# Kernel optimization log

Hardware: AMD Instinct MI355X
Metric: run time of the kernel (lower is better)

The kernel has to match this reference:

```python
import jax, jax.numpy as jnp
import numpy as np

N = 100000   # total nodes in batch
E = 200000   # total edges
G = 4000     # number of graphs
H = 128      # gin_size = gin_hidden = gin_mlp_hidden = linear_hidden
L = 2        # gin_layers


def setup_inputs() -> dict:
    key = jax.random.key(0)
    ks = jax.random.split(key, 24)
    rn = lambda i, shape, s=0.05: (jax.random.normal(ks[i], shape, jnp.float32) * s)
    inp = dict(
        x=rn(0, (N, 14), 1.0),
        edge_attr=rn(1, (E, 4), 1.0),
        edge_index=jax.random.randint(ks[2], (2, E), 0, N, dtype=jnp.int32),
        batch=jnp.sort(jax.random.randint(ks[3], (N,), 0, G, dtype=jnp.int32)),
        node_w=rn(4, (14, H)), node_b=jnp.zeros((H,), jnp.float32),
        edge_w=rn(5, (4, H)), edge_b=jnp.zeros((H,), jnp.float32),
        eps=jnp.zeros((L,), jnp.float32),
        gin_w1=rn(6, (L, H, H)), gin_b1=jnp.zeros((L, H), jnp.float32),
        gin_w2=rn(7, (L, H, H)), gin_b2=jnp.zeros((L, H), jnp.float32),
        em_w1=rn(8, (L, H, H)), em_b1=jnp.zeros((L, H), jnp.float32),
        em_w2=rn(9, (L, H, H)), em_b2=jnp.zeros((L, H), jnp.float32),
        gru_wih=rn(10, (3 * H, H)), gru_whh=rn(11, (3 * H, H)),
        gru_bih=jnp.zeros((3 * H,), jnp.float32), gru_bhh=jnp.zeros((3 * H,), jnp.float32),
        lstm_wih=rn(12, (4 * H, 2 * H)), lstm_whh=rn(13, (4 * H, H)),
        lstm_bih=jnp.zeros((4 * H,), jnp.float32), lstm_bhh=jnp.zeros((4 * H,), jnp.float32),
        fc_w1=rn(14, (2 * H, H)), fc_b1=jnp.zeros((H,), jnp.float32),
        fc_w2=rn(15, (H, 1)), fc_b2=jnp.zeros((1,), jnp.float32),
    )
    return inp


def reference(x, edge_attr, edge_index, batch,
              node_w, node_b, edge_w, edge_b, eps,
              gin_w1, gin_b1, gin_w2, gin_b2,
              em_w1, em_b1, em_w2, em_b2,
              gru_wih, gru_whh, gru_bih, gru_bhh,
              lstm_wih, lstm_whh, lstm_bih, lstm_bhh,
              fc_w1, fc_b1, fc_w2, fc_b2):
    src, dst = edge_index[0], edge_index[1]
    node = x @ node_w + node_b          # [N,H]
    edge = edge_attr @ edge_w + edge_b  # [E,H]
    h = node                            # GRU hidden state
    for l in range(L):
        # GINEConv: msg = relu(x_src + e), scatter-add to dst, (1+eps)*x + agg, then MLP
        msg = jax.nn.relu(node[src] + edge)                     # [E,H] gather
        agg = jax.ops.segment_sum(msg, dst, num_segments=N)     # [N,H] scatter-add
        z = (1.0 + eps[l]) * node + agg
        m = jax.nn.relu(z @ gin_w1[l] + gin_b1[l]) @ gin_w2[l] + gin_b2[l]
        # GRU cell (seq_len=1)
        gi = m @ gru_wih.T + gru_bih
        gh = h @ gru_whh.T + gru_bhh
        ir, iz, inn = jnp.split(gi, 3, axis=-1)
        hr, hz, hn = jnp.split(gh, 3, axis=-1)
        r = jax.nn.sigmoid(ir + hr)
        zt = jax.nn.sigmoid(iz + hz)
        n = jnp.tanh(inn + r * hn)
        h = (1.0 - zt) * n + zt * h
        node = h
        # edge feature update MLP
        edge = jax.nn.relu(edge @ em_w1[l] + em_b1[l]) @ em_w2[l] + em_b2[l]
    # Set2Set pooling, processing_steps=3
    qs = jnp.zeros((G, 2 * H), node.dtype)
    hl = jnp.zeros((G, H), node.dtype)
    cl = jnp.zeros((G, H), node.dtype)
    for _ in range(3):
        g = qs @ lstm_wih.T + lstm_bih + hl @ lstm_whh.T + lstm_bhh
        i_, f_, g_, o_ = jnp.split(g, 4, axis=-1)
        cl = jax.nn.sigmoid(f_) * cl + jax.nn.sigmoid(i_) * jnp.tanh(g_)
        hl = jax.nn.sigmoid(o_) * jnp.tanh(cl)
        q = hl                                                   # [G,H]
        e = jnp.sum(node * q[batch], axis=-1)                    # [N]
        emax = jax.ops.segment_max(e, batch, num_segments=G)
        ex = jnp.exp(e - emax[batch])
        denom = jax.ops.segment_sum(ex, batch, num_segments=G)
        a = ex / jnp.maximum(denom, 1e-9)[batch]                 # per-graph softmax
        r = jax.ops.segment_sum(a[:, None] * node, batch, num_segments=G)  # [G,H]
        qs = jnp.concatenate([q, r], axis=-1)                    # [G,2H]
    out = jax.nn.relu(qs @ fc_w1 + fc_b1) @ fc_w2 + fc_b2
    return out.reshape(-1)
```

## Files before the change

### kernel.cpp

```cpp
#include <hip/hip_runtime.h>
#include <hip/hip_bf16.h>

constexpr int TN = 100000;
constexpr int TE = 200000;
constexpr int TG = 4000;
constexpr int TH = 128;

using short8 = __attribute__((ext_vector_type(8))) short;
using f32x4  = __attribute__((ext_vector_type(4))) float;
typedef __hip_bfloat16 bf16;

#define DEVINL __device__ __forceinline__
DEVINL float sigm(float x)  { return 1.f / (1.f + __expf(-x)); }
DEVINL float ftanh(float x) { return 1.f - 2.f / (__expf(2.f * x) + 1.f); }
DEVINL void unpack8(uint4 v, float* f) {
    const ushort* u = (const ushort*)&v;
#pragma unroll
    for (int j = 0; j < 8; ++j) f[j] = __bfloat162float(*(const bf16*)&u[j]);
}

__global__ void conv6(const float* __restrict__ s0, const float* __restrict__ s1,
                      const float* __restrict__ s2, const float* __restrict__ s3,
                      const float* __restrict__ s4, const float* __restrict__ s5,
                      bf16* __restrict__ dst) {
    int i = blockIdx.x * 256 + threadIdx.x;
    if (i >= 6 * TH * TH) return;
    int m = i >> 14, r = i & 16383;
    int n = r >> 7, k = r & 127;
    const float* s = (m == 0) ? s0 : (m == 1) ? s1 : (m == 2) ? s2
                   : (m == 3) ? s3 : (m == 4) ? s4 : s5;
    dst[i] = __float2bfloat16(s[k * TH + n]);
}
__global__ void conv2(const float* __restrict__ a, const float* __restrict__ b,
                      bf16* __restrict__ dst) {
    int i = blockIdx.x * 256 + threadIdx.x;
    if (i >= 2 * 384 * TH) return;
    const float* s = (i < 384 * TH) ? a : b;
    int r = (i < 384 * TH) ? i : i - 384 * TH;
    dst[i] = __float2bfloat16(s[r]);
}
__global__ void convL(const float* __restrict__ wih, const float* __restrict__ whh,
                      bf16* __restrict__ dst) {
    int i = blockIdx.x * 256 + threadIdx.x;
    if (i >= 512 * 256) return;
    int c = i >> 8, k = i & 255;
    float v = (k < 128) ? wih[c * 256 + k] + whh[c * 128 + k] : wih[c * 256 + k];
    dst[i] = __float2bfloat16(v);
}

template<int K>
__global__ __launch_bounds__(256) void proj64(const float* __restrict__ X,
                                              const float* __restrict__ W,
                                              const float* __restrict__ b,
                                              ushort* __restrict__ out, int M) {
    __shared__ float xs[64][K];
    int tid = threadIdx.x;
    int bm = blockIdx.x * 64;
    for (int i = tid; i < 64 * K; i += 256) {
        int r = i / K, k = i % K;
        xs[r][k] = (bm + r < M) ? X[(size_t)(bm + r) * K + k] : 0.f;
    }
    __syncthreads();
    int rb = tid >> 4, h0 = (tid & 15) * 8;
    float acc[4][8];
#pragma unroll
    for (int j = 0; j < 4; ++j)
#pragma unroll
        for (int c = 0; c < 8; ++c) acc[j][c] = b[h0 + c];
#pragma unroll
    for (int k = 0; k < K; ++k) {
        float4 w0 = *(const float4*)(W + k * TH + h0);
        float4 w1 = *(const float4*)(W + k * TH + h0 + 4);
#pragma unroll
        for (int j = 0; j < 4; ++j) {
            float xv = xs[rb + 16 * j][k];
            acc[j][0] = fmaf(xv, w0.x, acc[j][0]); acc[j][1] = fmaf(xv, w0.y, acc[j][1]);
            acc[j][2] = fmaf(xv, w0.z, acc[j][2]); acc[j][3] = fmaf(xv, w0.w, acc[j][3]);
            acc[j][4] = fmaf(xv, w1.x, acc[j][4]); acc[j][5] = fmaf(xv, w1.y, acc[j][5]);
            acc[j][6] = fmaf(xv, w1.z, acc[j][6]); acc[j][7] = fmaf(xv, w1.w, acc[j][7]);
        }
    }
#pragma unroll
    for (int j = 0; j < 4; ++j) {
        int row = bm + rb + 16 * j;
        if (row >= M) continue;
        ushort o[8];
#pragma unroll
        for (int c = 0; c < 8; ++c) {
            bf16 v = __float2bfloat16(acc[j][c]);
            o[c] = *(ushort*)&v;
        }
        *(uint4*)(out + (size_t)row * TH + h0) = *(uint4*)o;
    }
}

__global__ __launch_bounds__(256) void proj_scatter(
    const float* __restrict__ X, const float* __restrict__ W,
    const float* __restrict__ b, const int* __restrict__ perm,
    ushort* __restrict__ out, int M) {
    __shared__ float xs[64][4];
    int tid = threadIdx.x;
    int bm = blockIdx.x * 64;
    if (tid < 64) {
        float4 a = make_float4(0.f, 0.f, 0.f, 0.f);
        if (bm + tid < M) a = *(const float4*)(X + (size_t)(bm + tid) * 4);
        xs[tid][0] = a.x; xs[tid][1] = a.y; xs[tid][2] = a.z; xs[tid][3] = a.w;
    }
    __syncthreads();
    int rb = tid >> 4, h0 = (tid & 15) * 8;
    float acc[4][8];
#pragma unroll
    for (int j = 0; j < 4; ++j)
#pragma unroll
        for (int c = 0; c < 8; ++c) acc[j][c] = b[h0 + c];
#pragma unroll
    for (int k = 0; k < 4; ++k) {
        float4 w0 = *(const float4*)(W + k * TH + h0);
        float4 w1 = *(const float4*)(W + k * TH + h0 + 4);
#pragma unroll
        for (int j = 0; j < 4; ++j) {
            float xv = xs[rb + 16 * j][k];
            acc[j][0] = fmaf(xv, w0.x, acc[j][0]); acc[j][1] = fmaf(xv, w0.y, acc[j][1]);
            acc[j][2] = fmaf(xv, w0.z, acc[j][2]); acc[j][3] = fmaf(xv, w0.w, acc[j][3]);
            acc[j][4] = fmaf(xv, w1.x, acc[j][4]); acc[j][5] = fmaf(xv, w1.y, acc[j][5]);
            acc[j][6] = fmaf(xv, w1.z, acc[j][6]); acc[j][7] = fmaf(xv, w1.w, acc[j][7]);
        }
    }
#pragma unroll
    for (int j = 0; j < 4; ++j) {
        int row = bm + rb + 16 * j;
        if (row >= M) continue;
        ushort o[8];
#pragma unroll
        for (int c = 0; c < 8; ++c) {
            bf16 v = __float2bfloat16(acc[j][c]);
            o[c] = *(ushort*)&v;
        }
        *(uint4*)(out + (size_t)perm[row] * TH + h0) = *(uint4*)o;
    }
}

__global__ void count_deg(const int* __restrict__ ei_dst, int* __restrict__ deg, int En) {
    int e = blockIdx.x * 256 + threadIdx.x;
    if (e < En) atomicAdd(&deg[ei_dst[e]], 1);
}
__global__ void scan_block(const int* __restrict__ deg, int* __restrict__ rowptr,
                           int* __restrict__ bsum, int Nn) {
    __shared__ int sm[256];
    int tid = threadIdx.x;
    int gid = blockIdx.x * 256 + tid;
    int v = (gid < Nn) ? deg[gid] : 0;
    int x = v;
    sm[tid] = x; __syncthreads();
    for (int off = 1; off < 256; off <<= 1) {
        int t = (tid >= off) ? sm[tid - off] : 0;
        __syncthreads();
        x += t; sm[tid] = x;
        __syncthreads();
    }
    if (gid < Nn) rowptr[gid] = x - v;
    if (tid == 255) bsum[blockIdx.x] = x;
}
__global__ void scan_bsum(const int* __restrict__ bsum, int* __restrict__ bsumx, int nb) {
    __shared__ int sm[512];
    int tid = threadIdx.x;
    int v = (tid < nb) ? bsum[tid] : 0;
    int x = v;
    sm[tid] = x; __syncthreads();
    for (int off = 1; off < 512; off <<= 1) {
        int t = (tid >= off) ? sm[tid - off] : 0;
        __syncthreads();
        x += t; sm[tid] = x;
        __syncthreads();
    }
    if (tid < nb) bsumx[tid] = x - v;
}
__global__ void add_off(int* __restrict__ rowptr, const int* __restrict__ bsumx,
                        int Nn, int Etot) {
    int gid = blockIdx.x * 256 + threadIdx.x;
    if (gid < Nn) rowptr[gid] += bsumx[gid >> 8];
    if (gid == 0) rowptr[Nn] = Etot;
}
__global__ void fill_csr(const int* __restrict__ ei_src, const int* __restrict__ ei_dst,
                         const int* __restrict__ rowptr, int* __restrict__ cur,
                         int* __restrict__ srcp, int* __restrict__ epos, int En) {
    int e = blockIdx.x * 256 + threadIdx.x;
    if (e >= En) return;
    int d = ei_dst[e];
    int p = atomicAdd(&cur[d], 1);
    int slot = rowptr[d] + p;
    srcp[slot] = ei_src[e];
    epos[e] = slot;
}
__global__ void build_gptr(const int* __restrict__ batch, int* __restrict__ gptr,
                           int Nn, int Gn) {
    int n = blockIdx.x * 256 + threadIdx.x;
    if (n >= Nn) return;
    int bc = batch[n];
    int bp = (n == 0) ? -1 : batch[n - 1];
    for (int g = bp + 1; g <= bc; ++g) gptr[g] = n;
    if (n == Nn - 1) for (int g = bc + 1; g <= Gn; ++g) gptr[g] = Nn;
}

__global__ __launch_bounds__(256) void aggregate_v8(
    const ushort* __restrict__ node, const ushort* __restrict__ ef,
    const int* __restrict__ srcp, const int* __restrict__ rowptr,
    const float* __restrict__ eps, int l, ushort* __restrict__ zb, int Nn) {
    int t = blockIdx.x * 256 + threadIdx.x;
    int n = t >> 4;
    if (n >= Nn) return;
    int c8 = (t & 15) * 8;
    float se = 1.f + eps[l];
    float acc[8];
    uint4 nv = *(const uint4*)(node + (size_t)n * TH + c8);
    unpack8(nv, acc);
#pragma unroll
    for (int j = 0; j < 8; ++j) acc[j] *= se;
    int s0 = rowptr[n], s1 = rowptr[n + 1];
    int i = s0;
    for (; i + 1 < s1; i += 2) {
        int sa = srcp[i], sb = srcp[i + 1];
        uint4 av0 = *(const uint4*)(node + (size_t)sa * TH + c8);
        uint4 bv0 = *(const uint4*)(ef + (size_t)i * TH + c8);
        uint4 av1 = *(const uint4*)(node + (size_t)sb * TH + c8);
        uint4 bv1 = *(const uint4*)(ef + (size_t)(i + 1) * TH + c8);
        float a0[8], b0[8], a1[8], b1[8];
        unpack8(av0, a0); unpack8(bv0, b0);
        unpack8(av1, a1); unpack8(bv1, b1);
#pragma unroll
        for (int j = 0; j < 8; ++j)
            acc[j] += fmaxf(a0[j] + b0[j], 0.f) + fmaxf(a1[j] + b1[j], 0.f);
    }
    if (i < s1) {
        int sa = srcp[i];
        uint4 av = *(const uint4*)(node + (size_t)sa * TH + c8);
        uint4 bv = *(const uint4*)(ef + (size_t)i * TH + c8);
        float af[8], bf[8];
        unpack8(av, af); unpack8(bv, bf);
#pragma unroll
        for (int j = 0; j < 8; ++j) acc[j] += fmaxf(af[j] + bf[j], 0.f);
    }
    ushort o[8];
#pragma unroll
    for (int j = 0; j < 8; ++j) {
        bf16 v = __float2bfloat16(acc[j]);
        o[j] = *(ushort*)&v;
    }
    *(uint4*)(zb + (size_t)n * TH + c8) = *(uint4*)o;
}

__global__ __launch_bounds__(256) void mlp2_fused(
    const ushort* __restrict__ A, const ushort* __restrict__ W1t,
    const float* __restrict__ b1, const ushort* __restrict__ W2t,
    const float* __restrict__ b2, ushort* __restrict__ C, int M)
{
    __shared__ ushort As[128 * 128];
    __shared__ ushort Ts[128 * 128];
    const int tid = threadIdx.x;
    const int bm = blockIdx.x * 128;
    const int lane = tid & 63, w = tid >> 6;
    const int lr = lane & 15, lq = lane >> 4;
    const int wm = (w & 1) * 64, wn = (w >> 1) * 64;
    short8 wf[4][4];
#pragma unroll
    for (int ni = 0; ni < 4; ++ni)
#pragma unroll
        for (int ks = 0; ks < 4; ++ks)
            wf[ni][ks] = *(const short8*)(W1t + (size_t)(wn + ni * 16 + lr) * 128 + ks * 32 + lq * 8);
#pragma unroll
    for (int p = 0; p < 8; ++p) {
        int ch = p * 256 + tid;
        int r = ch >> 4, c = ch & 15;
        int row = bm + r;
        uint4 v = make_uint4(0u, 0u, 0u, 0u);
        if (row < M) v = *(const uint4*)(A + (size_t)row * 128 + c * 8);
        *(uint4*)(&As[r * 128 + ((c ^ (r & 15)) * 8)]) = v;
    }
    __syncthreads();
    {
        f32x4 acc[4][4] = {};
#pragma unroll
        for (int ks = 0; ks < 4; ++ks) {
            int cb = ks * 4 + lq;
            short8 af[4];
#pragma unroll
            for (int mi = 0; mi < 4; ++mi)
                af[mi] = *(const short8*)(&As[(wm + mi * 16 + lr) * 128 + ((cb ^ lr) * 8)]);
#pragma unroll
            for (int mi = 0; mi < 4; ++mi)
#pragma unroll
                for (int ni = 0; ni < 4; ++ni)
                    acc[mi][ni] = __builtin_amdgcn_mfma_f32_16x16x32_bf16(af[mi], wf[ni][ks], acc[mi][ni], 0, 0, 0);
        }
#pragma unroll
        for (int mi = 0; mi < 4; ++mi)
#pragma unroll
            for (int reg = 0; reg < 4; ++reg) {
                int row = wm + mi * 16 + lq * 4 + reg;
#pragma unroll
                for (int ni = 0; ni < 4; ++ni) {
                    int col = wn + ni * 16 + lr;
                    float v = fmaxf(acc[mi][ni][reg] + b1[col], 0.f);
                    bf16 bv = __float2bfloat16(v);
                    Ts[row * 128 + (((col >> 3) ^ (row & 15)) * 8) + (col & 7)] = *(ushort*)&bv;
                }
            }
    }
#pragma unroll
    for (int ni = 0; ni < 4; ++ni)
#pragma unroll
        for (int ks = 0; ks < 4; ++ks)
            wf[ni][ks] = *(const short8*)(W2t + (size_t)(wn + ni * 16 + lr) * 128 + ks * 32 + lq * 8);
    __syncthreads();
    {
        f32x4 acc[4][4] = {};
#pragma unroll
        for (int ks = 0; ks < 4; ++ks) {
            int cb = ks * 4 + lq;
            short8 af[4];
#pragma unroll
            for (int mi = 0; mi < 4; ++mi)
                af[mi] = *(const short8*)(&Ts[(wm + mi * 16 + lr) * 128 + ((cb ^ lr) * 8)]);
#pragma unroll
            for (int mi = 0; mi < 4; ++mi)
#pragma unroll
                for (int ni = 0; ni < 4; ++ni)
                    acc[mi][ni] = __builtin_amdgcn_mfma_f32_16x16x32_bf16(af[mi], wf[ni][ks], acc[mi][ni], 0, 0, 0);
        }
#pragma unroll
        for (int mi = 0; mi < 4; ++mi)
#pragma unroll
            for (int reg = 0; reg < 4; ++reg) {
                int row = bm + wm + mi * 16 + lq * 4 + reg;
                if (row >= M) continue;
#pragma unroll
                for (int ni = 0; ni < 4; ++ni) {
                    int col = wn + ni * 16 + lr;
                    bf16 bv = __float2bfloat16(acc[mi][ni][reg] + b2[col]);
                    C[(size_t)row * 128 + col] = *(ushort*)&bv;
                }
            }
    }
}

__global__ __launch_bounds__(512, 4) void gru_fused(
    const ushort* __restrict__ mfeat, const ushort* __restrict__ wih,
    const ushort* __restrict__ whh, const float* __restrict__ bih,
    const float* __restrict__ bhh, ushort* __restrict__ node, int Nn)
{
    __shared__ ushort Ms[32 * 128];
    __shared__ ushort Hs[32 * 128];
    const int tid = threadIdx.x;
    const int bm = blockIdx.x * 32;
#pragma unroll
    for (int p = 0; p < 2; ++p) {
        int ch = p * 512 + tid;
        bool isH = ch >= 512;
        int r = (ch >> 4) & 31, c = ch & 15;
        int row = bm + r;
        uint4 v = make_uint4(0u, 0u, 0u, 0u);
        if (row < Nn) v = *(const uint4*)((isH ? node : mfeat) + (size_t)row * 128 + c * 8);
        ushort* dst = isH ? Hs : Ms;
        *(uint4*)(&dst[r * 128 + ((c ^ (r & 15)) * 8)]) = v;
    }
    const int lane = tid & 63, w = tid >> 6;
    const int lr = lane & 15, lq = lane >> 4;
    const int col = w * 16 + lr;
    auto loadw = [&](int ks, short8* wv) {
        int koff = ks * 32 + lq * 8;
        wv[0] = *(const short8*)(wih + (size_t)col * 128 + koff);
        wv[1] = *(const short8*)(wih + (size_t)(128 + col) * 128 + koff);
        wv[2] = *(const short8*)(wih + (size_t)(256 + col) * 128 + koff);
        wv[3] = *(const short8*)(whh + (size_t)col * 128 + koff);
        wv[4] = *(const short8*)(whh + (size_t)(128 + col) * 128 + koff);
        wv[5] = *(const short8*)(whh + (size_t)(256 + col) * 128 + koff);
    };
    short8 wA[6], wB[6];
    loadw(0, wA);
    __syncthreads();
    f32x4 aR[2] = {}, aZ[2] = {}, aN[2] = {}, aH[2] = {};
#pragma unroll
    for (int ks = 0; ks < 4; ++ks) {
        short8* cur = (ks & 1) ? wB : wA;
        short8* nxt = (ks & 1) ? wA : wB;
        if (ks < 3) loadw(ks + 1, nxt);
        int cb = ks * 4 + lq;
        short8 am[2], ah[2];
#pragma unroll
        for (int rt = 0; rt < 2; ++rt) {
            int off = (rt * 16 + lr) * 128 + ((cb ^ lr) * 8);
            am[rt] = *(const short8*)(&Ms[off]);
            ah[rt] = *(const short8*)(&Hs[off]);
        }
#pragma unroll
        for (int rt = 0; rt < 2; ++rt) {
            aR[rt] = __builtin_amdgcn_mfma_f32_16x16x32_bf16(am[rt], cur[0], aR[rt], 0, 0, 0);
            aR[rt] = __builtin_amdgcn_mfma_f32_16x16x32_bf16(ah[rt], cur[3], aR[rt], 0, 0, 0);
            aZ[rt] = __builtin_amdgcn_mfma_f32_16x16x32_bf16(am[rt], cur[1], aZ[rt], 0, 0, 0);
            aZ[rt] = __builtin_amdgcn_mfma_f32_16x16x32_bf16(ah[rt], cur[4], aZ[rt], 0, 0, 0);
            aN[rt] = __builtin_amdgcn_mfma_f32_16x16x32_bf16(am[rt], cur[2], aN[rt], 0, 0, 0);
            aH[rt] = __builtin_amdgcn_mfma_f32_16x16x32_bf16(ah[rt], cur[5], aH[rt], 0, 0, 0);
        }
    }
    {
        int h = col;
        float br = bih[h] + bhh[h];
        float bz = bih[128 + h] + bhh[128 + h];
        float bin = bih[256 + h], bhn = bhh[256 + h];
#pragma unroll
        for (int rt = 0; rt < 2; ++rt)
#pragma unroll
            for (int reg = 0; reg < 4; ++reg) {
                int lrow = rt * 16 + lq * 4 + reg;
                int row = bm + lrow;
                if (row >= Nn) continue;
                float r = sigm(aR[rt][reg] + br);
                float z = sigm(aZ[rt][reg] + bz);
                float n = ftanh(aN[rt][reg] + bin + r * (aH[rt][reg] + bhn));
                int hofs = lrow * 128 + (((h >> 3) ^ (lrow & 15)) * 8) + (h & 7);
                float hold = __bfloat162float(*(const bf16*)&Hs[hofs]);
                bf16 hv = __float2bfloat16((1.f - z) * n + z * hold);
                node[(size_t)row * 128 + h] = *(ushort*)&hv;
            }
    }
}

__global__ __launch_bounds__(256) void lstm_fused(
    ushort* __restrict__ s, const ushort* __restrict__ Wl,
    const float* __restrict__ bih, const float* __restrict__ bhh,
    float* __restrict__ cl, int Gn)
{
    __shared__ ushort Ss[32 * 256];
    const int tid = threadIdx.x;
    const int bm = blockIdx.x * 32;
#pragma unroll
    for (int p = 0; p < 4; ++p) {
        int ch = p * 256 + tid;
        int r = ch >> 5, c = ch & 31;
        int row = bm + r;
        uint4 v = make_uint4(0u, 0u, 0u, 0u);
        if (row < Gn) v = *(const uint4*)(s + (size_t)row * 256 + c * 8);
        *(uint4*)(&Ss[r * 256 + ((c ^ (r & 15)) * 8)]) = v;
    }
    __syncthreads();
    const int lane = tid & 63, w = tid >> 6;
    const int lr = lane & 15, lq = lane >> 4;
    f32x4 acc[2][4][2] = {};
#pragma unroll
    for (int ks = 0; ks < 8; ++ks) {
        int cb = ks * 4 + lq;
        short8 am[2];
#pragma unroll
        for (int rt = 0; rt < 2; ++rt)
            am[rt] = *(const short8*)(&Ss[(rt * 16 + lr) * 256 + ((cb ^ lr) * 8)]);
        int koff = ks * 32 + lq * 8;
#pragma unroll
        for (int g = 0; g < 4; ++g)
#pragma unroll
            for (int sub = 0; sub < 2; ++sub) {
                int col = g * 128 + w * 32 + sub * 16 + lr;
                short8 bf = *(const short8*)(Wl + (size_t)col * 256 + koff);
#pragma unroll
                for (int rt = 0; rt < 2; ++rt)
                    acc[rt][g][sub] = __builtin_amdgcn_mfma_f32_16x16x32_bf16(am[rt], bf, acc[rt][g][sub], 0, 0, 0);
            }
    }
#pragma unroll
    for (int sub = 0; sub < 2; ++sub) {
        int h = w * 32 + sub * 16 + lr;
        float bi = bih[h] + bhh[h];
        float bff = bih[128 + h] + bhh[128 + h];
        float bg = bih[256 + h] + bhh[256 + h];
        float bo = bih[384 + h] + bhh[384 + h];
#pragma unroll
        for (int rt = 0; rt < 2; ++rt)
#pragma unroll
            for (int reg = 0; reg < 4; ++reg) {
                int row = bm + rt * 16 + lq * 4 + reg;
                if (row >= Gn) continue;
                float iv = sigm(acc[rt][0][sub][reg] + bi);
                float fv = sigm(acc[rt][1][sub][reg] + bff);
                float gv = ftanh(acc[rt][2][sub][reg] + bg);
                float ov = sigm(acc[rt][3][sub][reg] + bo);
                float c = fv * cl[(size_t)row * 128 + h] + iv * gv;
                cl[(size_t)row * 128 + h] = c;
                bf16 hv = __float2bfloat16(ov * ftanh(c));
                s[(size_t)row * 256 + h] = *(ushort*)&hv;
            }
    }
}

__global__ __launch_bounds__(256) void att_fused(
    const ushort* __restrict__ node, ushort* __restrict__ s,
    const int* __restrict__ gptr)
{
    __shared__ float q[128];
    __shared__ float es[512];
    __shared__ float red[8];
    __shared__ float part[16][128];
    int g = blockIdx.x;
    int tid = threadIdx.x, lane = tid & 63, wid = tid >> 6;
    int n0 = gptr[g], n1 = gptr[g + 1];
    int cnt = n1 - n0; if (cnt > 512) cnt = 512;
    if (tid < 128) q[tid] = __bfloat162float(((const bf16*)s)[(size_t)g * 256 + tid]);
    __syncthreads();
    int gr = tid >> 4, c8 = (tid & 15) * 8;
    for (int i0 = 0; i0 < cnt; i0 += 16) {
        int i = i0 + gr;
        float p = 0.f;
        if (i < cnt) {
            uint4 v = *(const uint4*)(node + (size_t)(n0 + i) * TH + c8);
            float f[8]; unpack8(v, f);
#pragma unroll
            for (int j = 0; j < 8; ++j) p = fmaf(f[j], q[c8 + j], p);
        }
        p += __shfl_down(p, 8, 16);
        p += __shfl_down(p, 4, 16);
        p += __shfl_down(p, 2, 16);
        p += __shfl_down(p, 1, 16);
        if ((tid & 15) == 0 && i < cnt) es[i] = p;
    }
    __syncthreads();
    float m = -1e30f;
    for (int i = tid; i < cnt; i += 256) m = fmaxf(m, es[i]);
    for (int off = 32; off; off >>= 1) m = fmaxf(m, __shfl_down(m, off));
    if (lane == 0) red[wid] = m;
    __syncthreads();
    m = fmaxf(fmaxf(red[0], red[1]), fmaxf(red[2], red[3]));
    float sm = 0.f;
    for (int i = tid; i < cnt; i += 256) { float ex = __expf(es[i] - m); es[i] = ex; sm += ex; }
    for (int off = 32; off; off >>= 1) sm += __shfl_down(sm, off);
    if (lane == 0) red[4 + wid] = sm;
    __syncthreads();
    sm = red[4] + red[5] + red[6] + red[7];
    float inv = 1.f / fmaxf(sm, 1e-9f);
    float racc[8] = {};
    for (int i = gr; i < cnt; i += 16) {
        uint4 v = *(const uint4*)(node + (size_t)(n0 + i) * TH + c8);
        float f[8]; unpack8(v, f);
        float a = es[i];
#pragma unroll
        for (int j = 0; j < 8; ++j) racc[j] = fmaf(a, f[j], racc[j]);
    }
#pragma unroll
    for (int j = 0; j < 8; ++j) part[gr][c8 + j] = racc[j];
    __syncthreads();
    if (tid < 128) {
        float r = 0.f;
#pragma unroll
        for (int k = 0; k < 16; ++k) r += part[k][tid];
        bf16 rv = __float2bfloat16(r * inv);
        s[(size_t)g * 256 + 128 + tid] = *(ushort*)&rv;
    }
}

__global__ __launch_bounds__(128) void final_fc(const ushort* __restrict__ s,
                                                const float* __restrict__ w1,
                                                const float* __restrict__ b1,
                                                const float* __restrict__ w2,
                                                const float* __restrict__ b2,
                                                float* __restrict__ out) {
    __shared__ float q[256];
    __shared__ float red[2];
    int g = blockIdx.x, t = threadIdx.x;
    q[t] = __bfloat162float(((const bf16*)s)[(size_t)g * 256 + t]);
    q[t + 128] = __bfloat162float(((const bf16*)s)[(size_t)g * 256 + 128 + t]);
    __syncthreads();
    float acc = b1[t];
    for (int k = 0; k < 256; ++k) acc = fmaf(q[k], w1[k * TH + t], acc);
    acc = fmaxf(acc, 0.f);
    float p = acc * w2[t];
    for (int off = 32; off; off >>= 1) p += __shfl_down(p, off);
    if ((t & 63) == 0) red[t >> 6] = p;
    __syncthreads();
    if (t == 0) out[g] = red[0] + red[1] + b2[0];
}

static void launch_mlp2(const void* A, const bf16* W1t, const float* b1,
                        const bf16* W2t, const float* b2, void* C, int M, hipStream_t s) {
    hipLaunchKernelGGL(mlp2_fused, dim3((M + 127) / 128), dim3(256), 0, s,
                       (const ushort*)A, (const ushort*)W1t, b1, (const ushort*)W2t, b2,
                       (ushort*)C, M);
}

extern "C" void kernel_launch(void* const* d_in, const int* in_sizes, int n_in,
                              void* d_out, int out_size, void* d_ws, size_t ws_size,
                              hipStream_t stream) {
    const float* x         = (const float*)d_in[0];
    const float* edge_attr = (const float*)d_in[1];
    const int*   edge_index= (const int*)d_in[2];
    const int*   batch     = (const int*)d_in[3];
    const float* node_w    = (const float*)d_in[4];
    const float* node_b    = (const float*)d_in[5];
    const float* edge_w    = (const float*)d_in[6];
    const float* edge_b    = (const float*)d_in[7];
    const float* eps       = (const float*)d_in[8];
    const float* gin_w1    = (const float*)d_in[9];
    const float* gin_b1    = (const float*)d_in[10];
    const float* gin_w2    = (const float*)d_in[11];
    const float* gin_b2    = (const float*)d_in[12];
    const float* em_w1     = (const float*)d_in[13];
    const float* em_b1     = (const float*)d_in[14];
    const float* em_w2     = (const float*)d_in[15];
    const float* em_b2     = (const float*)d_in[16];
    const float* gru_wih   = (const float*)d_in[17];
    const float* gru_whh   = (const float*)d_in[18];
    const float* gru_bih   = (const float*)d_in[19];
    const float* gru_bhh   = (const float*)d_in[20];
    const float* lstm_wih  = (const float*)d_in[21];
    const float* lstm_whh  = (const float*)d_in[22];
    const float* lstm_bih  = (const float*)d_in[23];
    const float* lstm_bhh  = (const float*)d_in[24];
    const float* fc_w1     = (const float*)d_in[25];
    const float* fc_b1     = (const float*)d_in[26];
    const float* fc_w2     = (const float*)d_in[27];
    const float* fc_b2     = (const float*)d_in[28];
    float* out = (float*)d_out;
    const int* ei_src = edge_index;
    const int* ei_dst = edge_index + TE;

    char* base = (char*)d_ws;
    size_t off = 0;
    auto alloc = [&](size_t bytes) { void* p = base + off; off += (bytes + 15) & ~size_t(15); return p; };
    bf16*  nodeb = (bf16*)alloc((size_t)TN * TH * 2);
    bf16*  zb    = (bf16*)alloc((size_t)TN * TH * 2);
    bf16*  e1b   = (bf16*)alloc((size_t)TE * TH * 2);
    int*   deg   = (int*)alloc((size_t)TN * 4);
    int*   rowptr= (int*)alloc((size_t)(TN + 1) * 4);
    int*   cur   = (int*)alloc((size_t)TN * 4);
    int*   srcp  = (int*)alloc((size_t)TE * 4);
    int*   epos  = (int*)alloc((size_t)TE * 4);
    int*   bsum  = (int*)alloc(512 * 4);
    int*   bsumx = (int*)alloc(512 * 4);
    int*   gptr  = (int*)alloc((size_t)(TG + 1) * 4);
    bf16*  w6    = (bf16*)alloc(6 * TH * TH * 2);
    bf16*  wgru  = (bf16*)alloc(2 * 384 * TH * 2);
    bf16*  wl    = (bf16*)alloc(512 * 256 * 2);
    if (ws_size < off) return;

    bf16* w_gin1_0 = w6;
    bf16* w_gin1_1 = w6 + 1 * TH * TH;
    bf16* w_gin2_0 = w6 + 2 * TH * TH;
    bf16* w_gin2_1 = w6 + 3 * TH * TH;
    bf16* w_em1    = w6 + 4 * TH * TH;
    bf16* w_em2    = w6 + 5 * TH * TH;
    bf16* w_wih    = wgru;
    bf16* w_whh    = wgru + 384 * TH;

    ushort* sbuf = (ushort*)e1b;
    float*  cl   = (float*)(sbuf + (size_t)TG * 256);

    hipMemsetAsync(deg, 0, (size_t)TN * 4, stream);
    hipMemsetAsync(cur, 0, (size_t)TN * 4, stream);
    count_deg<<<(TE + 255) / 256, 256, 0, stream>>>(ei_dst, deg, TE);
    int nb = (TN + 255) / 256;
    scan_block<<<nb, 256, 0, stream>>>(deg, rowptr, bsum, TN);
    scan_bsum<<<1, 512, 0, stream>>>(bsum, bsumx, nb);
    add_off<<<nb, 256, 0, stream>>>(rowptr, bsumx, TN, TE);
    fill_csr<<<(TE + 255) / 256, 256, 0, stream>>>(ei_src, ei_dst, rowptr, cur, srcp, epos, TE);
    build_gptr<<<(TN + 255) / 256, 256, 0, stream>>>(batch, gptr, TN, TG);

    conv6<<<(6 * TH * TH + 255) / 256, 256, 0, stream>>>(
        gin_w1, gin_w1 + TH * TH, gin_w2, gin_w2 + TH * TH, em_w1, em_w2, w6);
    conv2<<<(2 * 384 * TH + 255) / 256, 256, 0, stream>>>(gru_wih, gru_whh, wgru);
    convL<<<(512 * 256 + 255) / 256, 256, 0, stream>>>(lstm_wih, lstm_whh, wl);

    proj64<14><<<(TN + 63) / 64, 256, 0, stream>>>(x, node_w, node_b, (ushort*)nodeb, TN);
    proj_scatter<<<(TE + 63) / 64, 256, 0, stream>>>(edge_attr, edge_w, edge_b,
                                                     epos, (ushort*)e1b, TE);

    aggregate_v8<<<(TN * 16 + 255) / 256, 256, 0, stream>>>(
        (const ushort*)nodeb, (const ushort*)e1b, srcp, rowptr, eps, 0, (ushort*)zb, TN);
    launch_mlp2(zb, w_gin1_0, gin_b1, w_gin2_0, gin_b2, zb, TN, stream);
    gru_fused<<<(TN + 31) / 32, 512, 0, stream>>>(
        (const ushort*)zb, (const ushort*)w_wih, (const ushort*)w_whh,
        gru_bih, gru_bhh, (ushort*)nodeb, TN);

    launch_mlp2(e1b, w_em1, em_b1, w_em2, em_b2, e1b, TE, stream);
    aggregate_v8<<<(TN * 16 + 255) / 256, 256, 0, stream>>>(
        (const ushort*)nodeb, (const ushort*)e1b, srcp, rowptr, eps, 1, (ushort*)zb, TN);
    launch_mlp2(zb, w_gin1_1, gin_b1 + TH, w_gin2_1, gin_b2 + TH, zb, TN, stream);
    gru_fused<<<(TN + 31) / 32, 512, 0, stream>>>(
        (const ushort*)zb, (const ushort*)w_wih, (const ushort*)w_whh,
        gru_bih, gru_bhh, (ushort*)nodeb, TN);

    hipMemsetAsync(sbuf, 0, (size_t)TG * 256 * 2 + (size_t)TG * 128 * 4, stream);
    for (int st = 0; st < 3; ++st) {
        lstm_fused<<<(TG + 31) / 32, 256, 0, stream>>>(
            sbuf, (const ushort*)wl, lstm_bih, lstm_bhh, cl, TG);
        att_fused<<<TG, 256, 0, stream>>>((const ushort*)nodeb, sbuf, gptr);
    }

    final_fc<<<TG, 128, 0, stream>>>(sbuf, fc_w1, fc_b1, fc_w2, fc_b2, out);
}
```

Baseline: 621.3 us.

## Merge weight conversions, enlarge GRU row tile, shrink LSTM row tile

```diff
diff --git a/kernel.cpp b/kernel.cpp
--- a/kernel.cpp
+++ b/kernel.cpp
@@ -19,33 +19,35 @@
     for (int j = 0; j < 8; ++j) f[j] = __bfloat162float(*(const bf16*)&u[j]);
 }
 
-__global__ void conv6(const float* __restrict__ s0, const float* __restrict__ s1,
-                      const float* __restrict__ s2, const float* __restrict__ s3,
-                      const float* __restrict__ s4, const float* __restrict__ s5,
-                      bf16* __restrict__ dst) {
+__global__ void convAll(const float* __restrict__ g1, const float* __restrict__ g2,
+                        const float* __restrict__ e1, const float* __restrict__ e2,
+                        const float* __restrict__ gwih, const float* __restrict__ gwhh,
+                        const float* __restrict__ lwih, const float* __restrict__ lwhh,
+                        bf16* __restrict__ w6, bf16* __restrict__ wgru,
+                        bf16* __restrict__ wl) {
     int i = blockIdx.x * 256 + threadIdx.x;
-    if (i >= 6 * TH * TH) return;
-    int m = i >> 14, r = i & 16383;
-    int n = r >> 7, k = r & 127;
-    const float* s = (m == 0) ? s0 : (m == 1) ? s1 : (m == 2) ? s2
-                   : (m == 3) ? s3 : (m == 4) ? s4 : s5;
-    dst[i] = __float2bfloat16(s[k * TH + n]);
-}
-__global__ void conv2(const float* __restrict__ a, const float* __restrict__ b,
-                      bf16* __restrict__ dst) {
-    int i = blockIdx.x * 256 + threadIdx.x;
-    if (i >= 2 * 384 * TH) return;
-    const float* s = (i < 384 * TH) ? a : b;
-    int r = (i < 384 * TH) ? i : i - 384 * TH;
-    dst[i] = __float2bfloat16(s[r]);
-}
-__global__ void convL(const float* __restrict__ wih, const float* __restrict__ whh,
-                      bf16* __restrict__ dst) {
-    int i = blockIdx.x * 256 + threadIdx.x;
-    if (i >= 512 * 256) return;
-    int c = i >> 8, k = i & 255;
-    float v = (k < 128) ? wih[c * 256 + k] + whh[c * 128 + k] : wih[c * 256 + k];
-    dst[i] = __float2bfloat16(v);
+    if (i < 6 * TH * TH) {
+        int m = i >> 14, r = i & 16383;
+        int n = r >> 7, k = r & 127;
+        const float* s = (m == 0) ? g1 : (m == 1) ? g1 + TH * TH
+                       : (m == 2) ? g2 : (m == 3) ? g2 + TH * TH
+                       : (m == 4) ? e1 : e2;
+        w6[i] = __float2bfloat16(s[k * TH + n]);
+        return;
+    }
+    i -= 6 * TH * TH;
+    if (i < 2 * 384 * TH) {
+        const float* s = (i < 384 * TH) ? gwih : gwhh;
+        int r = (i < 384 * TH) ? i : i - 384 * TH;
+        wgru[i] = __float2bfloat16(s[r]);
+        return;
+    }
+    i -= 2 * 384 * TH;
+    if (i < 512 * 256) {
+        int c = i >> 8, k = i & 255;
+        float v = (k < 128) ? lwih[c * 256 + k] + lwhh[c * 128 + k] : lwih[c * 256 + k];
+        wl[i] = __float2bfloat16(v);
+    }
 }
 
 template<int K>
@@ -348,58 +350,47 @@
     const ushort* __restrict__ whh, const float* __restrict__ bih,
     const float* __restrict__ bhh, ushort* __restrict__ node, int Nn)
 {
-    __shared__ ushort Ms[32 * 128];
-    __shared__ ushort Hs[32 * 128];
+    __shared__ ushort Ms[64 * 128];
+    __shared__ ushort Hs[64 * 128];
     const int tid = threadIdx.x;
-    const int bm = blockIdx.x * 32;
-#pragma unroll
-    for (int p = 0; p < 2; ++p) {
+    const int bm = blockIdx.x * 64;
+#pragma unroll
+    for (int p = 0; p < 4; ++p) {
         int ch = p * 512 + tid;
-        bool isH = ch >= 512;
-        int r = (ch >> 4) & 31, c = ch & 15;
+        bool isH = ch >= 1024;
+        int r = (ch >> 4) & 63, c = ch & 15;
         int row = bm + r;
         uint4 v = make_uint4(0u, 0u, 0u, 0u);
         if (row < Nn) v = *(const uint4*)((isH ? node : mfeat) + (size_t)row * 128 + c * 8);
         ushort* dst = isH ? Hs : Ms;
         *(uint4*)(&dst[r * 128 + ((c ^ (r & 15)) * 8)]) = v;
     }
+    __syncthreads();
     const int lane = tid & 63, w = tid >> 6;
     const int lr = lane & 15, lq = lane >> 4;
     const int col = w * 16 + lr;
-    auto loadw = [&](int ks, short8* wv) {
+    f32x4 aR[4] = {}, aZ[4] = {}, aN[4] = {}, aH[4] = {};
+#pragma unroll
+    for (int ks = 0; ks < 4; ++ks) {
         int koff = ks * 32 + lq * 8;
-        wv[0] = *(const short8*)(wih + (size_t)col * 128 + koff);
-        wv[1] = *(const short8*)(wih + (size_t)(128 + col) * 128 + koff);
-        wv[2] = *(const short8*)(wih + (size_t)(256 + col) * 128 + koff);
-        wv[3] = *(const short8*)(whh + (size_t)col * 128 + koff);
-        wv[4] = *(const short8*)(whh + (size_t)(128 + col) * 128 + koff);
-        wv[5] = *(const short8*)(whh + (size_t)(256 + col) * 128 + koff);
-    };
-    short8 wA[6], wB[6];
-    loadw(0, wA);
-    __syncthreads();
-    f32x4 aR[2] = {}, aZ[2] = {}, aN[2] = {}, aH[2] = {};
-#pragma unroll
-    for (int ks = 0; ks < 4; ++ks) {
-        short8* cur = (ks & 1) ? wB : wA;
-        short8* nxt = (ks & 1) ? wA : wB;
-        if (ks < 3) loadw(ks + 1, nxt);
+        short8 wv0 = *(const short8*)(wih + (size_t)col * 128 + koff);
+        short8 wv1 = *(const short8*)(wih + (size_t)(128 + col) * 128 + koff);
+        short8 wv2 = *(const short8*)(wih + (size_t)(256 + col) * 128 + koff);
+        short8 wv3 = *(const short8*)(whh + (size_t)col * 128 + koff);
+        short8 wv4 = *(const short8*)(whh + (size_t)(128 + col) * 128 + koff);
+        short8 wv5 = *(const short8*)(whh + (size_t)(256 + col) * 128 + koff);
         int cb = ks * 4 + lq;
-        short8 am[2], ah[2];
-#pragma unroll
-        for (int rt = 0; rt < 2; ++rt) {
+#pragma unroll
+        for (int rt = 0; rt < 4; ++rt) {
             int off = (rt * 16 + lr) * 128 + ((cb ^ lr) * 8);
-            am[rt] = *(const short8*)(&Ms[off]);
-            ah[rt] = *(const short8*)(&Hs[off]);
-        }
-#pragma unroll
-        for (int rt = 0; rt < 2; ++rt) {
-            aR[rt] = __builtin_amdgcn_mfma_f32_16x16x32_bf16(am[rt], cur[0], aR[rt], 0, 0, 0);
-            aR[rt] = __builtin_amdgcn_mfma_f32_16x16x32_bf16(ah[rt], cur[3], aR[rt], 0, 0, 0);
-            aZ[rt] = __builtin_amdgcn_mfma_f32_16x16x32_bf16(am[rt], cur[1], aZ[rt], 0, 0, 0);
-            aZ[rt] = __builtin_amdgcn_mfma_f32_16x16x32_bf16(ah[rt], cur[4], aZ[rt], 0, 0, 0);
-            aN[rt] = __builtin_amdgcn_mfma_f32_16x16x32_bf16(am[rt], cur[2], aN[rt], 0, 0, 0);
-            aH[rt] = __builtin_amdgcn_mfma_f32_16x16x32_bf16(ah[rt], cur[5], aH[rt], 0, 0, 0);
+            short8 am = *(const short8*)(&Ms[off]);
+            short8 ah = *(const short8*)(&Hs[off]);
+            aR[rt] = __builtin_amdgcn_mfma_f32_16x16x32_bf16(am, wv0, aR[rt], 0, 0, 0);
+            aR[rt] = __builtin_amdgcn_mfma_f32_16x16x32_bf16(ah, wv3, aR[rt], 0, 0, 0);
+            aZ[rt] = __builtin_amdgcn_mfma_f32_16x16x32_bf16(am, wv1, aZ[rt], 0, 0, 0);
+            aZ[rt] = __builtin_amdgcn_mfma_f32_16x16x32_bf16(ah, wv4, aZ[rt], 0, 0, 0);
+            aN[rt] = __builtin_amdgcn_mfma_f32_16x16x32_bf16(am, wv2, aN[rt], 0, 0, 0);
+            aH[rt] = __builtin_amdgcn_mfma_f32_16x16x32_bf16(ah, wv5, aH[rt], 0, 0, 0);
         }
     }
     {
@@ -408,7 +399,7 @@
         float bz = bih[128 + h] + bhh[128 + h];
         float bin = bih[256 + h], bhn = bhh[256 + h];
 #pragma unroll
-        for (int rt = 0; rt < 2; ++rt)
+        for (int rt = 0; rt < 4; ++rt)
 #pragma unroll
             for (int reg = 0; reg < 4; ++reg) {
                 int lrow = rt * 16 + lq * 4 + reg;
@@ -430,11 +421,11 @@
     const float* __restrict__ bih, const float* __restrict__ bhh,
     float* __restrict__ cl, int Gn)
 {
-    __shared__ ushort Ss[32 * 256];
+    __shared__ ushort Ss[16 * 256];
     const int tid = threadIdx.x;
-    const int bm = blockIdx.x * 32;
-#pragma unroll
-    for (int p = 0; p < 4; ++p) {
+    const int bm = blockIdx.x * 16;
+#pragma unroll
+    for (int p = 0; p < 2; ++p) {
         int ch = p * 256 + tid;
         int r = ch >> 5, c = ch & 31;
         int row = bm + r;
@@ -445,14 +436,11 @@
     __syncthreads();
     const int lane = tid & 63, w = tid >> 6;
     const int lr = lane & 15, lq = lane >> 4;
-    f32x4 acc[2][4][2] = {};
+    f32x4 acc[4][2] = {};
 #pragma unroll
     for (int ks = 0; ks < 8; ++ks) {
         int cb = ks * 4 + lq;
-        short8 am[2];
-#pragma unroll
-        for (int rt = 0; rt < 2; ++rt)
-            am[rt] = *(const short8*)(&Ss[(rt * 16 + lr) * 256 + ((cb ^ lr) * 8)]);
+        short8 am = *(const short8*)(&Ss[lr * 256 + ((cb ^ lr) * 8)]);
         int koff = ks * 32 + lq * 8;
 #pragma unroll
         for (int g = 0; g < 4; ++g)
@@ -460,9 +448,7 @@
             for (int sub = 0; sub < 2; ++sub) {
                 int col = g * 128 + w * 32 + sub * 16 + lr;
                 short8 bf = *(const short8*)(Wl + (size_t)col * 256 + koff);
-#pragma unroll
-                for (int rt = 0; rt < 2; ++rt)
-                    acc[rt][g][sub] = __builtin_amdgcn_mfma_f32_16x16x32_bf16(am[rt], bf, acc[rt][g][sub], 0, 0, 0);
+                acc[g][sub] = __builtin_amdgcn_mfma_f32_16x16x32_bf16(am, bf, acc[g][sub], 0, 0, 0);
             }
     }
 #pragma unroll
@@ -473,20 +459,18 @@
         float bg = bih[256 + h] + bhh[256 + h];
         float bo = bih[384 + h] + bhh[384 + h];
 #pragma unroll
-        for (int rt = 0; rt < 2; ++rt)
-#pragma unroll
-            for (int reg = 0; reg < 4; ++reg) {
-                int row = bm + rt * 16 + lq * 4 + reg;
-                if (row >= Gn) continue;
-                float iv = sigm(acc[rt][0][sub][reg] + bi);
-                float fv = sigm(acc[rt][1][sub][reg] + bff);
-                float gv = ftanh(acc[rt][2][sub][reg] + bg);
-                float ov = sigm(acc[rt][3][sub][reg] + bo);
-                float c = fv * cl[(size_t)row * 128 + h] + iv * gv;
-                cl[(size_t)row * 128 + h] = c;
-                bf16 hv = __float2bfloat16(ov * ftanh(c));
-                s[(size_t)row * 256 + h] = *(ushort*)&hv;
-            }
+        for (int reg = 0; reg < 4; ++reg) {
+            int row = bm + lq * 4 + reg;
+            if (row >= Gn) continue;
+            float iv = sigm(acc[0][sub][reg] + bi);
+            float fv = sigm(acc[1][sub][reg] + bff);
+            float gv = ftanh(acc[2][sub][reg] + bg);
+            float ov = sigm(acc[3][sub][reg] + bo);
+            float c = fv * cl[(size_t)row * 128 + h] + iv * gv;
+            cl[(size_t)row * 128 + h] = c;
+            bf16 hv = __float2bfloat16(ov * ftanh(c));
+            s[(size_t)row * 256 + h] = *(ushort*)&hv;
+        }
     }
 }
 
@@ -660,10 +644,10 @@
     fill_csr<<<(TE + 255) / 256, 256, 0, stream>>>(ei_src, ei_dst, rowptr, cur, srcp, epos, TE);
     build_gptr<<<(TN + 255) / 256, 256, 0, stream>>>(batch, gptr, TN, TG);
 
-    conv6<<<(6 * TH * TH + 255) / 256, 256, 0, stream>>>(
-        gin_w1, gin_w1 + TH * TH, gin_w2, gin_w2 + TH * TH, em_w1, em_w2, w6);
-    conv2<<<(2 * 384 * TH + 255) / 256, 256, 0, stream>>>(gru_wih, gru_whh, wgru);
-    convL<<<(512 * 256 + 255) / 256, 256, 0, stream>>>(lstm_wih, lstm_whh, wl);
+    int convTot = 6 * TH * TH + 2 * 384 * TH + 512 * 256;
+    convAll<<<(convTot + 255) / 256, 256, 0, stream>>>(
+        gin_w1, gin_w2, em_w1, em_w2, gru_wih, gru_whh, lstm_wih, lstm_whh,
+        w6, wgru, wl);
 
     proj64<14><<<(TN + 63) / 64, 256, 0, stream>>>(x, node_w, node_b, (ushort*)nodeb, TN);
     proj_scatter<<<(TE + 63) / 64, 256, 0, stream>>>(edge_attr, edge_w, edge_b,
@@ -672,7 +656,7 @@
     aggregate_v8<<<(TN * 16 + 255) / 256, 256, 0, stream>>>(
         (const ushort*)nodeb, (const ushort*)e1b, srcp, rowptr, eps, 0, (ushort*)zb, TN);
     launch_mlp2(zb, w_gin1_0, gin_b1, w_gin2_0, gin_b2, zb, TN, stream);
-    gru_fused<<<(TN + 31) / 32, 512, 0, stream>>>(
+    gru_fused<<<(TN + 63) / 64, 512, 0, stream>>>(
         (const ushort*)zb, (const ushort*)w_wih, (const ushort*)w_whh,
         gru_bih, gru_bhh, (ushort*)nodeb, TN);
 
@@ -680,13 +664,13 @@
     aggregate_v8<<<(TN * 16 + 255) / 256, 256, 0, stream>>>(
         (const ushort*)nodeb, (const ushort*)e1b, srcp, rowptr, eps, 1, (ushort*)zb, TN);
     launch_mlp2(zb, w_gin1_1, gin_b1 + TH, w_gin2_1, gin_b2 + TH, zb, TN, stream);
-    gru_fused<<<(TN + 31) / 32, 512, 0, stream>>>(
+    gru_fused<<<(TN + 63) / 64, 512, 0, stream>>>(
         (const ushort*)zb, (const ushort*)w_wih, (const ushort*)w_whh,
         gru_bih, gru_bhh, (ushort*)nodeb, TN);
 
     hipMemsetAsync(sbuf, 0, (size_t)TG * 256 * 2 + (size_t)TG * 128 * 4, stream);
     for (int st = 0; st < 3; ++st) {
-        lstm_fused<<<(TG + 31) / 32, 256, 0, stream>>>(
+        lstm_fused<<<(TG + 15) / 16, 256, 0, stream>>>(
             sbuf, (const ushort*)wl, lstm_bih, lstm_bhh, cl, TG);
         att_fused<<<TG, 256, 0, stream>>>((const ushort*)nodeb, sbuf, gptr);
     }
```

Result: faster. 556.9 us, median of 2 (-10.4%).
